# Kernel optimization log

Measured on AMD Instinct MI355X. Metric: run time of the kernel, lower is better.

Reference implementation:

```python
import jax, jax.numpy as jnp
import numpy as np

Q, N, FDIM, HDIM = 4096, 1024, 64, 128


def setup_inputs() -> dict:
    key = jax.random.key(0)
    ks = jax.random.split(key, 7)
    s = 0.05
    return {
        "query_points": jax.random.normal(ks[0], (Q, 3), dtype=jnp.float32),
        "node_features": jax.random.normal(ks[1], (N, FDIM), dtype=jnp.float32),
        "node_positions": jax.random.normal(ks[2], (N, 3), dtype=jnp.float32),
        # attention MLP: Linear(F+3 -> H), ReLU, Linear(H -> 1)
        "aW1": jax.random.normal(ks[3], (FDIM + 3, HDIM), dtype=jnp.float32) * s,
        "ab1": jnp.zeros((HDIM,), dtype=jnp.float32),
        "aW2": jax.random.normal(ks[4], (HDIM, 1), dtype=jnp.float32) * s,
        "ab2": jnp.zeros((1,), dtype=jnp.float32),
        # decoder MLP: Linear(F -> H), ReLU, Linear(H -> 3)
        "dW1": jax.random.normal(ks[5], (FDIM, HDIM), dtype=jnp.float32) * s,
        "db1": jnp.zeros((HDIM,), dtype=jnp.float32),
        "dW2": jax.random.normal(ks[6], (HDIM, 3), dtype=jnp.float32) * s,
        "db2": jnp.zeros((3,), dtype=jnp.float32),
    }


def reference(query_points, node_features, node_positions,
              aW1, ab1, aW2, ab2, dW1, db1, dW2, db2):
    F = node_features.shape[1]
    # pairwise offsets: [Q, N, 3]
    diff = query_points[:, None, :] - node_positions[None, :, :]
    # xy-plane distance -> inverse-distance weights: [Q, N, 1]
    dist = jnp.linalg.norm(diff[..., :2], axis=-1, keepdims=True)
    w = 1.0 / (dist + 1e-6)
    # attn MLP on concat([node_features, diff]); split W1 so the feature
    # part ([N,F]@[F,H]) is computed once instead of per query pair.
    h = jax.nn.relu(node_features @ aW1[:F] + diff @ aW1[F:] + ab1)  # [Q, N, H]
    score = h @ aW2 + ab2                                            # [Q, N, 1]
    attn = jax.nn.softmax(score * w, axis=1)                         # [Q, N, 1]
    agg = jnp.einsum('qn,nf->qf', attn[..., 0], node_features)       # [Q, F]
    return jax.nn.relu(agg @ dW1 + db1) @ dW2 + db2                  # [Q, 3]
```

## Files before the change

kernel.cpp:

```cpp
#include <hip/hip_runtime.h>
#include <math.h>

#define QN 4096
#define NN 1024
#define FD 64
#define HD 128

typedef float v2f __attribute__((ext_vector_type(2)));

#define OFF_UB    0
#define OFF_B     524288
#define OFF_VU    655360
#define OFF_VB    659456
#define OFF_L     660480
#define OFF_PM    4854784
#define OFF_PART  5116928
#define OFF_SPART 7214080

__global__ __launch_bounds__(256) void k0_prep(
    const float* __restrict__ qp, const float* __restrict__ nf,
    const float* __restrict__ npos, const float* __restrict__ aW1,
    const float* __restrict__ ab1, const float* __restrict__ aW2,
    float* __restrict__ B, float* __restrict__ UB,
    float* __restrict__ vu, float* __restrict__ vb) {
  int bid = blockIdx.x, t = threadIdx.x;
  if (bid < 2048) {
    int idx = bid * 256 + t;
    int e = idx & 1, lane = (idx >> 1) & 63, qq = (idx >> 7) & 3;
    int h2 = (idx >> 9) & 63, qblk = idx >> 15;
    int q = qblk * 256 + qq * 64 + lane;
    int h = h2 * 2 + e;
    float u = qp[q*3+0] * aW1[(FD+0)*HD + h]
            + qp[q*3+1] * aW1[(FD+1)*HD + h]
            + qp[q*3+2] * aW1[(FD+2)*HD + h];
    UB[idx] = u;
  } else if (bid < 2560) {
    int i2 = (bid - 2048) * 256 + t;
    int n = i2 >> 7, h = i2 & 127;
    float s = ab1[h];
    #pragma unroll
    for (int f = 0; f < FD; ++f) s = fmaf(nf[n*FD+f], aW1[f*HD+h], s);
    s -= npos[n*3+0] * aW1[(FD+0)*HD + h]
       + npos[n*3+1] * aW1[(FD+1)*HD + h]
       + npos[n*3+2] * aW1[(FD+2)*HD + h];
    B[i2] = s;
    float pv = s * aW2[h];
    #pragma unroll
    for (int m = 1; m < 64; m <<= 1) pv += __shfl_xor(pv, m, 64);
    __shared__ float ps[4];
    if ((t & 63) == 0) ps[t >> 6] = pv;
    __syncthreads();
    if (t == 0)   vb[n] = ps[0] + ps[1];
    if (t == 128) vb[n] = ps[2] + ps[3];
  } else {
    int q = (bid - 2560) * 256 + t;
    float q0 = qp[q*3+0], q1 = qp[q*3+1], q2 = qp[q*3+2];
    float acc = 0.f;
    #pragma unroll
    for (int h = 0; h < HD; ++h) {
      float u = q0 * aW1[(FD+0)*HD + h]
              + q1 * aW1[(FD+1)*HD + h]
              + q2 * aW1[(FD+2)*HD + h];
      acc = fmaf(aW2[h], u, acc);
    }
    vu[q] = acc;
  }
}


#define LOADU(dst) { \
  _Pragma("unroll") for (int qq = 0; qq < 4; ++qq) { \
    dst[qq][0] = P0[qq*64]; \
    dst[qq][1] = P0[qq*64 + 256]; \
    dst[qq][2] = P1[qq*64]; \
    dst[qq][3] = P1[qq*64 + 256]; } \
  P0 += 1024; P1 += 1024; }

#define COMPUTE(u) { \
  float aw0 = aw[0], aw1 = aw[1], aw2 = aw[2], aw3 = aw[3]; \
  float aw4 = aw[4], aw5 = aw[5], aw6 = aw[6], aw7 = aw[7]; \
  _Pragma("unroll") for (int nn = 0; nn < 4; ++nn) { \
    v2f b0 = bsB[nn*64], b1 = bsB[nn*64 + 1]; \
    v2f b2 = bsB[nn*64 + 2], b3 = bsB[nn*64 + 3]; \
    _Pragma("unroll") for (int qq = 0; qq < 4; ++qq) { \
      v2f t0 = u[qq][0] + b0; \
      v2f t1 = u[qq][1] + b1; \
      v2f t2 = u[qq][2] + b2; \
      v2f t3 = u[qq][3] + b3; \
      float a = acc[qq][nn]; \
      a = fmaf(aw0, __builtin_fabsf(t0.x), a); \
      a = fmaf(aw1, __builtin_fabsf(t0.y), a); \
      a = fmaf(aw2, __builtin_fabsf(t1.x), a); \
      a = fmaf(aw3, __builtin_fabsf(t1.y), a); \
      a = fmaf(aw4, __builtin_fabsf(t2.x), a); \
      a = fmaf(aw5, __builtin_fabsf(t2.y), a); \
      a = fmaf(aw6, __builtin_fabsf(t3.x), a); \
      a = fmaf(aw7, __builtin_fabsf(t3.y), a); \
      acc[qq][nn] = a; } } \
  bsB += 4; aw += 8; }

__global__ __launch_bounds__(256) void k2_logits(
    const float* __restrict__ Bg, const float* __restrict__ UB,
    const float* __restrict__ aW2, const float* __restrict__ ab2,
    const float* __restrict__ qp, const float* __restrict__ npos,
    const float* __restrict__ vu, const float* __restrict__ vb,
    float* __restrict__ L, float* __restrict__ pm) {
  __shared__ float Bs[16 * HD];
  __shared__ float red[4][4][64];
  const int q0 = blockIdx.x * 256, n0 = blockIdx.y * 16;
  const int t = threadIdx.x;
  {
    const float4* src = (const float4*)(Bg + n0 * HD);
    float4* dst = (float4*)Bs;
    #pragma unroll
    for (int r = 0; r < 2; ++r) dst[r*256 + t] = src[r*256 + t];
  }
  __syncthreads();
  const int lane = t & 63, w = t >> 6;
  const int nb = w * 4;

  float acc[4][4];
  #pragma unroll
  for (int qq = 0; qq < 4; ++qq)
    #pragma unroll
    for (int nn = 0; nn < 4; ++nn) acc[qq][nn] = 0.f;

  const v2f* P0 = (const v2f*)UB + (size_t)blockIdx.x * 16384 + lane;
  const v2f* P1 = P0 + 512;
  const v2f* bsB = (const v2f*)Bs + nb * 64;
  const float* aw = aW2;

  v2f uA[4][4], uB4[4][4];
  LOADU(uA);
  #pragma unroll 1
  for (int hc = 0; hc < 14; hc += 2) {
    LOADU(uB4);
    COMPUTE(uA);
    LOADU(uA);
    COMPUTE(uB4);
  }
  LOADU(uB4);
  COMPUTE(uA);
  COMPUTE(uB4);

  const float bias2 = ab2[0];
  float qx[4], qy[4], vuq[4], m4[4];
  #pragma unroll
  for (int qq = 0; qq < 4; ++qq) {
    int q = q0 + qq*64 + lane;
    qx[qq] = qp[q*3+0];
    qy[qq] = qp[q*3+1];
    vuq[qq] = vu[q];
    m4[qq] = -3.4e38f;
  }
  #pragma unroll
  for (int nn = 0; nn < 4; ++nn) {
    int n = n0 + nb + nn;
    float px = npos[n*3+0], py = npos[n*3+1];
    float vbn = vb[n];
    #pragma unroll
    for (int qq = 0; qq < 4; ++qq) {
      float dx = qx[qq] - px, dy = qy[qq] - py;
      float wgt = 1.f / (sqrtf(dx*dx + dy*dy) + 1e-6f);
      float score = fmaf(0.5f, vuq[qq] + vbn + acc[qq][nn], bias2);
      float lg = score * wgt;
      L[n * QN + q0 + qq*64 + lane] = lg;
      m4[qq] = fmaxf(m4[qq], lg);
    }
  }
  #pragma unroll
  for (int qq = 0; qq < 4; ++qq) red[w][qq][lane] = m4[qq];
  __syncthreads();
  {
    int qq = t >> 6, ll = t & 63;
    float mm = fmaxf(fmaxf(red[0][qq][ll], red[1][qq][ll]),
                     fmaxf(red[2][qq][ll], red[3][qq][ll]));
    pm[blockIdx.y * QN + q0 + qq*64 + ll] = mm;
  }
}

__global__ __launch_bounds__(256) void k4_agg(
    const float* __restrict__ L, const float* __restrict__ pm,
    const float* __restrict__ nf, float* __restrict__ part,
    float* __restrict__ spart) {
  __shared__ float red[4][2][32][33];
  __shared__ float sred[4][33];
  int b = blockIdx.x;
  int qt = b & 127, c = b >> 7;
  int t = threadIdx.x, lane = t & 63, w = t >> 6;
  int qi = lane & 31, fh = lane >> 5;
  int q = qt * 32 + qi;

  float m = -3.4e38f;
  #pragma unroll
  for (int k = 0; k < 64; ++k) m = fmaxf(m, pm[k * QN + q]);

  float acc[32];
  #pragma unroll
  for (int f = 0; f < 32; ++f) acc[f] = 0.f;
  float s = 0.f;

  int nbase = c * 128 + w * 32;
  const float* Lp = L + (size_t)nbase * QN + q;
  float cur = *Lp;
  for (int i = 0; i < 32; ++i) {
    float nxt = (i < 31) ? Lp[(size_t)(i + 1) * QN] : 0.f;
    float p = exp2f((cur - m) * 1.44269504088896f);
    s += p;
    const float4* nfr = (const float4*)(nf + (nbase + i) * FD + fh * 32);
    #pragma unroll
    for (int g = 0; g < 8; ++g) {
      float4 a = nfr[g];
      acc[g*4+0] = fmaf(p, a.x, acc[g*4+0]);
      acc[g*4+1] = fmaf(p, a.y, acc[g*4+1]);
      acc[g*4+2] = fmaf(p, a.z, acc[g*4+2]);
      acc[g*4+3] = fmaf(p, a.w, acc[g*4+3]);
    }
    cur = nxt;
  }

  #pragma unroll
  for (int fi = 0; fi < 32; ++fi) red[w][fh][fi][qi] = acc[fi];
  if (fh == 0) sred[w][qi] = s;
  __syncthreads();
  #pragma unroll
  for (int k = 0; k < 8; ++k) {
    int idx = k * 256 + t;
    int qq = idx >> 6, f = idx & 63;
    int f1 = f >> 5, f0 = f & 31;
    float sum = red[0][f1][f0][qq] + red[1][f1][f0][qq]
              + red[2][f1][f0][qq] + red[3][f1][f0][qq];
    part[((size_t)c * QN + qt*32 + qq) * 64 + f] = sum;
  }
  if (t < 32) {
    spart[c * QN + qt*32 + t] = sred[0][t] + sred[1][t] + sred[2][t] + sred[3][t];
  }
}

__global__ __launch_bounds__(256) void k5_dec(
    const float* __restrict__ part, const float* __restrict__ spart,
    const float* __restrict__ dW1, const float* __restrict__ db1,
    const float* __restrict__ dW2, const float* __restrict__ db2,
    float* __restrict__ out) {
  __shared__ float agg[16][64];
  __shared__ float inv[16];
  __shared__ float h1s[16][128];
  int t = threadIdx.x;
  int qb = blockIdx.x * 16;
  if (t < 16) {
    float s = 0.f;
    #pragma unroll
    for (int c = 0; c < 8; ++c) s += spart[c*QN + qb + t];
    inv[t] = 1.f / s;
  }
  {
    int f = t & 63, qh = t >> 6;
    #pragma unroll
    for (int pass = 0; pass < 4; ++pass) {
      int qs = pass*4 + qh;
      float v = 0.f;
      #pragma unroll
      for (int c = 0; c < 8; ++c) v += part[((size_t)c*QN + qb + qs)*64 + f];
      agg[qs][f] = v;
    }
  }
  __syncthreads();
  {
    int h = t & 127, qg = t >> 7;
    #pragma unroll
    for (int k = 0; k < 8; ++k) {
      int qs = qg*8 + k;
      float a = 0.f;
      #pragma unroll
      for (int f = 0; f < 64; ++f) a = fmaf(agg[qs][f], dW1[f*HD + h], a);
      h1s[qs][h] = fmaxf(a * inv[qs] + db1[h], 0.f);
    }
  }
  __syncthreads();
  if (t < 48) {
    int qs = t / 3, o = t % 3;
    float a = db2[o];
    #pragma unroll
    for (int h = 0; h < HD; ++h) a = fmaf(h1s[qs][h], dW2[h*3 + o], a);
    out[(qb + qs)*3 + o] = a;
  }
}

extern "C" void kernel_launch(void* const* d_in, const int* in_sizes, int n_in,
                              void* d_out, int out_size, void* d_ws, size_t ws_size,
                              hipStream_t stream) {
  const float* qp   = (const float*)d_in[0];
  const float* nf   = (const float*)d_in[1];
  const float* npos = (const float*)d_in[2];
  const float* aW1  = (const float*)d_in[3];
  const float* ab1  = (const float*)d_in[4];
  const float* aW2  = (const float*)d_in[5];
  const float* ab2  = (const float*)d_in[6];
  const float* dW1  = (const float*)d_in[7];
  const float* db1  = (const float*)d_in[8];
  const float* dW2  = (const float*)d_in[9];
  const float* db2  = (const float*)d_in[10];

  float* ws    = (float*)d_ws;
  float* UB    = ws + OFF_UB;
  float* B     = ws + OFF_B;
  float* vu    = ws + OFF_VU;
  float* vb    = ws + OFF_VB;
  float* L     = ws + OFF_L;
  float* pm    = ws + OFF_PM;
  float* part  = ws + OFF_PART;
  float* spart = ws + OFF_SPART;

  hipLaunchKernelGGL(k0_prep, dim3(2576), dim3(256), 0, stream,
                     qp, nf, npos, aW1, ab1, aW2, B, UB, vu, vb);
  hipLaunchKernelGGL(k2_logits, dim3(16, 64), dim3(256), 0, stream,
                     B, UB, aW2, ab2, qp, npos, vu, vb, L, pm);
  hipLaunchKernelGGL(k4_agg, dim3(1024), dim3(256), 0, stream, L, pm, nf, part, spart);
  hipLaunchKernelGGL(k5_dec, dim3(256), dim3(256), 0, stream,
                     part, spart, dW1, db1, dW2, db2, (float*)d_out);
}
```

Before: 104.3 us.

## Retile logits kernel to one query per thread with scalar B loads

The U table is re-laid out as h-pair-major over all queries. Each thread now owns one query and 16 nodes, instead of a 4x4 query-by-node tile fed from an LDS copy of B. B values are read directly from global memory at wave-uniform addresses, which the compiler can turn into scalar loads, removing the LDS staging, the syncthreads and the cross-wave max reduction. This trades B reuse across the query tile for cheaper broadcast loads, and each thread reads U for only one query per h step instead of four.

New measurement: 107.3 us. 2.8% more time.

```diff
diff --git a/kernel.cpp b/kernel.cpp
--- a/kernel.cpp
+++ b/kernel.cpp
@@ -8,7 +8,7 @@
 
 typedef float v2f __attribute__((ext_vector_type(2)));
 
-#define OFF_UB    0
+#define OFF_UT2   0
 #define OFF_B     524288
 #define OFF_VU    655360
 #define OFF_VB    659456
@@ -21,19 +21,17 @@
     const float* __restrict__ qp, const float* __restrict__ nf,
     const float* __restrict__ npos, const float* __restrict__ aW1,
     const float* __restrict__ ab1, const float* __restrict__ aW2,
-    float* __restrict__ B, float* __restrict__ UB,
+    float* __restrict__ B, float* __restrict__ UT2,
     float* __restrict__ vu, float* __restrict__ vb) {
   int bid = blockIdx.x, t = threadIdx.x;
   if (bid < 2048) {
     int idx = bid * 256 + t;
-    int e = idx & 1, lane = (idx >> 1) & 63, qq = (idx >> 7) & 3;
-    int h2 = (idx >> 9) & 63, qblk = idx >> 15;
-    int q = qblk * 256 + qq * 64 + lane;
+    int e = idx & 1, q = (idx >> 1) & 4095, h2 = idx >> 13;
     int h = h2 * 2 + e;
     float u = qp[q*3+0] * aW1[(FD+0)*HD + h]
             + qp[q*3+1] * aW1[(FD+1)*HD + h]
             + qp[q*3+2] * aW1[(FD+2)*HD + h];
-    UB[idx] = u;
+    UT2[idx] = u;
   } else if (bid < 2560) {
     int i2 = (bid - 2048) * 256 + t;
     int n = i2 >> 7, h = i2 & 127;
@@ -67,116 +65,74 @@
   }
 }
 
-
-#define LOADU(dst) { \
-  _Pragma("unroll") for (int qq = 0; qq < 4; ++qq) { \
-    dst[qq][0] = P0[qq*64]; \
-    dst[qq][1] = P0[qq*64 + 256]; \
-    dst[qq][2] = P1[qq*64]; \
-    dst[qq][3] = P1[qq*64 + 256]; } \
-  P0 += 1024; P1 += 1024; }
-
-#define COMPUTE(u) { \
-  float aw0 = aw[0], aw1 = aw[1], aw2 = aw[2], aw3 = aw[3]; \
-  float aw4 = aw[4], aw5 = aw[5], aw6 = aw[6], aw7 = aw[7]; \
-  _Pragma("unroll") for (int nn = 0; nn < 4; ++nn) { \
-    v2f b0 = bsB[nn*64], b1 = bsB[nn*64 + 1]; \
-    v2f b2 = bsB[nn*64 + 2], b3 = bsB[nn*64 + 3]; \
-    _Pragma("unroll") for (int qq = 0; qq < 4; ++qq) { \
-      v2f t0 = u[qq][0] + b0; \
-      v2f t1 = u[qq][1] + b1; \
-      v2f t2 = u[qq][2] + b2; \
-      v2f t3 = u[qq][3] + b3; \
-      float a = acc[qq][nn]; \
-      a = fmaf(aw0, __builtin_fabsf(t0.x), a); \
-      a = fmaf(aw1, __builtin_fabsf(t0.y), a); \
-      a = fmaf(aw2, __builtin_fabsf(t1.x), a); \
-      a = fmaf(aw3, __builtin_fabsf(t1.y), a); \
-      a = fmaf(aw4, __builtin_fabsf(t2.x), a); \
-      a = fmaf(aw5, __builtin_fabsf(t2.y), a); \
-      a = fmaf(aw6, __builtin_fabsf(t3.x), a); \
-      a = fmaf(aw7, __builtin_fabsf(t3.y), a); \
-      acc[qq][nn] = a; } } \
-  bsB += 4; aw += 8; }
-
 __global__ __launch_bounds__(256) void k2_logits(
-    const float* __restrict__ Bg, const float* __restrict__ UB,
+    const float* __restrict__ Bg, const float* __restrict__ UT2,
     const float* __restrict__ aW2, const float* __restrict__ ab2,
     const float* __restrict__ qp, const float* __restrict__ npos,
     const float* __restrict__ vu, const float* __restrict__ vb,
     float* __restrict__ L, float* __restrict__ pm) {
-  __shared__ float Bs[16 * HD];
-  __shared__ float red[4][4][64];
-  const int q0 = blockIdx.x * 256, n0 = blockIdx.y * 16;
   const int t = threadIdx.x;
-  {
-    const float4* src = (const float4*)(Bg + n0 * HD);
-    float4* dst = (float4*)Bs;
-    #pragma unroll
-    for (int r = 0; r < 2; ++r) dst[r*256 + t] = src[r*256 + t];
-  }
-  __syncthreads();
   const int lane = t & 63, w = t >> 6;
-  const int nb = w * 4;
-
-  float acc[4][4];
-  #pragma unroll
-  for (int qq = 0; qq < 4; ++qq)
-    #pragma unroll
-    for (int nn = 0; nn < 4; ++nn) acc[qq][nn] = 0.f;
-
-  const v2f* P0 = (const v2f*)UB + (size_t)blockIdx.x * 16384 + lane;
-  const v2f* P1 = P0 + 512;
-  const v2f* bsB = (const v2f*)Bs + nb * 64;
-  const float* aw = aW2;
-
-  v2f uA[4][4], uB4[4][4];
-  LOADU(uA);
+  const int q = blockIdx.x * 256 + w * 64 + lane;
+  const int n0 = blockIdx.y * 16;
+
+  float acc[16];
+  #pragma unroll
+  for (int nn = 0; nn < 16; ++nn) acc[nn] = 0.f;
+
+  const v2f* up = (const v2f*)UT2 + q;
+
+  v2f uc[4], un[4];
+  #pragma unroll
+  for (int p = 0; p < 4; ++p) uc[p] = up[p * 4096];
+
   #pragma unroll 1
-  for (int hc = 0; hc < 14; hc += 2) {
-    LOADU(uB4);
-    COMPUTE(uA);
-    LOADU(uA);
-    COMPUTE(uB4);
-  }
-  LOADU(uB4);
-  COMPUTE(uA);
-  COMPUTE(uB4);
+  for (int hc = 0; hc < 16; ++hc) {
+    if (hc < 15) {
+      const v2f* upn = up + (hc + 1) * 4 * 4096;
+      #pragma unroll
+      for (int p = 0; p < 4; ++p) un[p] = upn[p * 4096];
+    }
+    const float* awp = aW2 + hc * 8;
+    float aw0 = awp[0], aw1 = awp[1], aw2 = awp[2], aw3 = awp[3];
+    float aw4 = awp[4], aw5 = awp[5], aw6 = awp[6], aw7 = awp[7];
+    #pragma unroll
+    for (int nn = 0; nn < 16; ++nn) {
+      const float* bp = Bg + (n0 + nn) * HD + hc * 8;
+      float b0 = bp[0], b1 = bp[1], b2 = bp[2], b3 = bp[3];
+      float b4 = bp[4], b5 = bp[5], b6 = bp[6], b7 = bp[7];
+      float a = acc[nn];
+      a = fmaf(aw0, __builtin_fabsf(uc[0].x + b0), a);
+      a = fmaf(aw1, __builtin_fabsf(uc[0].y + b1), a);
+      a = fmaf(aw2, __builtin_fabsf(uc[1].x + b2), a);
+      a = fmaf(aw3, __builtin_fabsf(uc[1].y + b3), a);
+      a = fmaf(aw4, __builtin_fabsf(uc[2].x + b4), a);
+      a = fmaf(aw5, __builtin_fabsf(uc[2].y + b5), a);
+      a = fmaf(aw6, __builtin_fabsf(uc[3].x + b6), a);
+      a = fmaf(aw7, __builtin_fabsf(uc[3].y + b7), a);
+      acc[nn] = a;
+    }
+    #pragma unroll
+    for (int p = 0; p < 4; ++p) uc[p] = un[p];
+  }
 
   const float bias2 = ab2[0];
-  float qx[4], qy[4], vuq[4], m4[4];
-  #pragma unroll
-  for (int qq = 0; qq < 4; ++qq) {
-    int q = q0 + qq*64 + lane;
-    qx[qq] = qp[q*3+0];
-    qy[qq] = qp[q*3+1];
-    vuq[qq] = vu[q];
-    m4[qq] = -3.4e38f;
-  }
-  #pragma unroll
-  for (int nn = 0; nn < 4; ++nn) {
-    int n = n0 + nb + nn;
+  const float qx = qp[q*3+0], qy = qp[q*3+1];
+  const float vuq = vu[q];
+  float m = -3.4e38f;
+  #pragma unroll
+  for (int nn = 0; nn < 16; ++nn) {
+    int n = n0 + nn;
     float px = npos[n*3+0], py = npos[n*3+1];
     float vbn = vb[n];
-    #pragma unroll
-    for (int qq = 0; qq < 4; ++qq) {
-      float dx = qx[qq] - px, dy = qy[qq] - py;
-      float wgt = 1.f / (sqrtf(dx*dx + dy*dy) + 1e-6f);
-      float score = fmaf(0.5f, vuq[qq] + vbn + acc[qq][nn], bias2);
-      float lg = score * wgt;
-      L[n * QN + q0 + qq*64 + lane] = lg;
-      m4[qq] = fmaxf(m4[qq], lg);
-    }
-  }
-  #pragma unroll
-  for (int qq = 0; qq < 4; ++qq) red[w][qq][lane] = m4[qq];
-  __syncthreads();
-  {
-    int qq = t >> 6, ll = t & 63;
-    float mm = fmaxf(fmaxf(red[0][qq][ll], red[1][qq][ll]),
-                     fmaxf(red[2][qq][ll], red[3][qq][ll]));
-    pm[blockIdx.y * QN + q0 + qq*64 + ll] = mm;
-  }
+    float dx = qx - px, dy = qy - py;
+    float wgt = 1.f / (sqrtf(dx*dx + dy*dy) + 1e-6f);
+    float score = fmaf(0.5f, vuq + vbn + acc[nn], bias2);
+    float lg = score * wgt;
+    L[n * QN + q] = lg;
+    m = fmaxf(m, lg);
+  }
+  pm[blockIdx.y * QN + q] = m;
 }
 
 __global__ __launch_bounds__(256) void k4_agg(
@@ -302,7 +258,7 @@
   const float* db2  = (const float*)d_in[10];
 
   float* ws    = (float*)d_ws;
-  float* UB    = ws + OFF_UB;
+  float* UT2   = ws + OFF_UT2;
   float* B     = ws + OFF_B;
   float* vu    = ws + OFF_VU;
   float* vb    = ws + OFF_VB;
@@ -312,9 +268,9 @@
   float* spart = ws + OFF_SPART;
 
   hipLaunchKernelGGL(k0_prep, dim3(2576), dim3(256), 0, stream,
-                     qp, nf, npos, aW1, ab1, aW2, B, UB, vu, vb);
+                     qp, nf, npos, aW1, ab1, aW2, B, UT2, vu, vb);
   hipLaunchKernelGGL(k2_logits, dim3(16, 64), dim3(256), 0, stream,
-                     B, UB, aW2, ab2, qp, npos, vu, vb, L, pm);
+                     B, UT2, aW2, ab2, qp, npos, vu, vb, L, pm);
   hipLaunchKernelGGL(k4_agg, dim3(1024), dim3(256), 0, stream, L, pm, nf, part, spart);
   hipLaunchKernelGGL(k5_dec, dim3(256), dim3(256), 0, stream,
                      part, spart, dW1, db1, dW2, db2, (float*)d_out);
```

## Repack query projection as h4-major float4 layout and deepen logit prefetch

Applied to the files above, without the earlier changes.

Changes the per-query projection buffer to a layout with four consecutive hidden units per float4, so the logits kernel issues 16-byte loads instead of 8-byte ones and reads B from shared memory as float4. Packed adds are emitted through inline v_pk_add_f32 asm, and the aW2 values are now read per use instead of cached in locals. The aggregation kernel now prefetches logits four rows ahead instead of one to hide global-load latency. Risks include more register pressure, and the inline asm may block compiler scheduling.

Result: no change. 105.0 us (+0.6%).

```diff
diff --git a/kernel.cpp b/kernel.cpp
--- a/kernel.cpp
+++ b/kernel.cpp
@@ -7,8 +7,9 @@
 #define HD 128
 
 typedef float v2f __attribute__((ext_vector_type(2)));
-
-#define OFF_UB    0
+typedef float v4f __attribute__((ext_vector_type(4)));
+
+#define OFF_UT4   0
 #define OFF_B     524288
 #define OFF_VU    655360
 #define OFF_VB    659456
@@ -21,19 +22,17 @@
     const float* __restrict__ qp, const float* __restrict__ nf,
     const float* __restrict__ npos, const float* __restrict__ aW1,
     const float* __restrict__ ab1, const float* __restrict__ aW2,
-    float* __restrict__ B, float* __restrict__ UB,
+    float* __restrict__ B, float* __restrict__ UT4,
     float* __restrict__ vu, float* __restrict__ vb) {
   int bid = blockIdx.x, t = threadIdx.x;
   if (bid < 2048) {
     int idx = bid * 256 + t;
-    int e = idx & 1, lane = (idx >> 1) & 63, qq = (idx >> 7) & 3;
-    int h2 = (idx >> 9) & 63, qblk = idx >> 15;
-    int q = qblk * 256 + qq * 64 + lane;
-    int h = h2 * 2 + e;
+    int j = idx & 3, q = (idx >> 2) & 4095, h4 = idx >> 14;
+    int h = h4 * 4 + j;
     float u = qp[q*3+0] * aW1[(FD+0)*HD + h]
             + qp[q*3+1] * aW1[(FD+1)*HD + h]
             + qp[q*3+2] * aW1[(FD+2)*HD + h];
-    UB[idx] = u;
+    UT4[idx] = u;
   } else if (bid < 2560) {
     int i2 = (bid - 2048) * 256 + t;
     int n = i2 >> 7, h = i2 & 127;
@@ -67,40 +66,44 @@
   }
 }
 
-
 #define LOADU(dst) { \
   _Pragma("unroll") for (int qq = 0; qq < 4; ++qq) { \
-    dst[qq][0] = P0[qq*64]; \
-    dst[qq][1] = P0[qq*64 + 256]; \
-    dst[qq][2] = P1[qq*64]; \
-    dst[qq][3] = P1[qq*64 + 256]; } \
-  P0 += 1024; P1 += 1024; }
+    dst[qq][0] = p0[qq*64]; \
+    dst[qq][1] = p1[qq*64]; } \
+  p0 += 8192; p1 += 8192; }
 
 #define COMPUTE(u) { \
-  float aw0 = aw[0], aw1 = aw[1], aw2 = aw[2], aw3 = aw[3]; \
-  float aw4 = aw[4], aw5 = aw[5], aw6 = aw[6], aw7 = aw[7]; \
   _Pragma("unroll") for (int nn = 0; nn < 4; ++nn) { \
-    v2f b0 = bsB[nn*64], b1 = bsB[nn*64 + 1]; \
-    v2f b2 = bsB[nn*64 + 2], b3 = bsB[nn*64 + 3]; \
+    v4f b0 = bsb[(nb + nn)*32]; \
+    v4f b1 = bsb[(nb + nn)*32 + 1]; \
+    v2f b01 = __builtin_shufflevector(b0, b0, 0, 1); \
+    v2f b23 = __builtin_shufflevector(b0, b0, 2, 3); \
+    v2f b45 = __builtin_shufflevector(b1, b1, 0, 1); \
+    v2f b67 = __builtin_shufflevector(b1, b1, 2, 3); \
     _Pragma("unroll") for (int qq = 0; qq < 4; ++qq) { \
-      v2f t0 = u[qq][0] + b0; \
-      v2f t1 = u[qq][1] + b1; \
-      v2f t2 = u[qq][2] + b2; \
-      v2f t3 = u[qq][3] + b3; \
+      v2f u01 = __builtin_shufflevector(u[qq][0], u[qq][0], 0, 1); \
+      v2f u23 = __builtin_shufflevector(u[qq][0], u[qq][0], 2, 3); \
+      v2f u45 = __builtin_shufflevector(u[qq][1], u[qq][1], 0, 1); \
+      v2f u67 = __builtin_shufflevector(u[qq][1], u[qq][1], 2, 3); \
+      v2f t0, t1, t2, t3; \
+      asm("v_pk_add_f32 %0, %1, %2" : "=v"(t0) : "v"(u01), "v"(b01)); \
+      asm("v_pk_add_f32 %0, %1, %2" : "=v"(t1) : "v"(u23), "v"(b23)); \
+      asm("v_pk_add_f32 %0, %1, %2" : "=v"(t2) : "v"(u45), "v"(b45)); \
+      asm("v_pk_add_f32 %0, %1, %2" : "=v"(t3) : "v"(u67), "v"(b67)); \
       float a = acc[qq][nn]; \
-      a = fmaf(aw0, __builtin_fabsf(t0.x), a); \
-      a = fmaf(aw1, __builtin_fabsf(t0.y), a); \
-      a = fmaf(aw2, __builtin_fabsf(t1.x), a); \
-      a = fmaf(aw3, __builtin_fabsf(t1.y), a); \
-      a = fmaf(aw4, __builtin_fabsf(t2.x), a); \
-      a = fmaf(aw5, __builtin_fabsf(t2.y), a); \
-      a = fmaf(aw6, __builtin_fabsf(t3.x), a); \
-      a = fmaf(aw7, __builtin_fabsf(t3.y), a); \
+      a = fmaf(aw[0], __builtin_fabsf(t0.x), a); \
+      a = fmaf(aw[1], __builtin_fabsf(t0.y), a); \
+      a = fmaf(aw[2], __builtin_fabsf(t1.x), a); \
+      a = fmaf(aw[3], __builtin_fabsf(t1.y), a); \
+      a = fmaf(aw[4], __builtin_fabsf(t2.x), a); \
+      a = fmaf(aw[5], __builtin_fabsf(t2.y), a); \
+      a = fmaf(aw[6], __builtin_fabsf(t3.x), a); \
+      a = fmaf(aw[7], __builtin_fabsf(t3.y), a); \
       acc[qq][nn] = a; } } \
-  bsB += 4; aw += 8; }
+  bsb += 2; aw += 8; }
 
 __global__ __launch_bounds__(256) void k2_logits(
-    const float* __restrict__ Bg, const float* __restrict__ UB,
+    const float* __restrict__ Bg, const float* __restrict__ UT4,
     const float* __restrict__ aW2, const float* __restrict__ ab2,
     const float* __restrict__ qp, const float* __restrict__ npos,
     const float* __restrict__ vu, const float* __restrict__ vb,
@@ -125,12 +128,12 @@
     #pragma unroll
     for (int nn = 0; nn < 4; ++nn) acc[qq][nn] = 0.f;
 
-  const v2f* P0 = (const v2f*)UB + (size_t)blockIdx.x * 16384 + lane;
-  const v2f* P1 = P0 + 512;
-  const v2f* bsB = (const v2f*)Bs + nb * 64;
+  const v4f* p0 = (const v4f*)UT4 + q0 + lane;
+  const v4f* p1 = p0 + 4096;
+  const v4f* bsb = (const v4f*)Bs;
   const float* aw = aW2;
 
-  v2f uA[4][4], uB4[4][4];
+  v4f uA[4][2], uB4[4][2];
   LOADU(uA);
   #pragma unroll 1
   for (int hc = 0; hc < 14; hc += 2) {
@@ -202,9 +205,15 @@
 
   int nbase = c * 128 + w * 32;
   const float* Lp = L + (size_t)nbase * QN + q;
-  float cur = *Lp;
+
+  float pre[4];
+  #pragma unroll
+  for (int j = 0; j < 4; ++j) pre[j] = Lp[(size_t)j * QN];
+
+  #pragma unroll 4
   for (int i = 0; i < 32; ++i) {
-    float nxt = (i < 31) ? Lp[(size_t)(i + 1) * QN] : 0.f;
+    float cur = pre[i & 3];
+    if (i < 28) pre[i & 3] = Lp[(size_t)(i + 4) * QN];
     float p = exp2f((cur - m) * 1.44269504088896f);
     s += p;
     const float4* nfr = (const float4*)(nf + (nbase + i) * FD + fh * 32);
@@ -216,7 +225,6 @@
       acc[g*4+2] = fmaf(p, a.z, acc[g*4+2]);
       acc[g*4+3] = fmaf(p, a.w, acc[g*4+3]);
     }
-    cur = nxt;
   }
 
   #pragma unroll
@@ -302,7 +310,7 @@
   const float* db2  = (const float*)d_in[10];
 
   float* ws    = (float*)d_ws;
-  float* UB    = ws + OFF_UB;
+  float* UT4   = ws + OFF_UT4;
   float* B     = ws + OFF_B;
   float* vu    = ws + OFF_VU;
   float* vb    = ws + OFF_VB;
@@ -312,9 +320,9 @@
   float* spart = ws + OFF_SPART;
 
   hipLaunchKernelGGL(k0_prep, dim3(2576), dim3(256), 0, stream,
-                     qp, nf, npos, aW1, ab1, aW2, B, UB, vu, vb);
+                     qp, nf, npos, aW1, ab1, aW2, B, UT4, vu, vb);
   hipLaunchKernelGGL(k2_logits, dim3(16, 64), dim3(256), 0, stream,
-                     B, UB, aW2, ab2, qp, npos, vu, vb, L, pm);
+                     B, UT4, aW2, ab2, qp, npos, vu, vb, L, pm);
   hipLaunchKernelGGL(k4_agg, dim3(1024), dim3(256), 0, stream, L, pm, nf, part, spart);
   hipLaunchKernelGGL(k5_dec, dim3(256), dim3(256), 0, stream,
                      part, spart, dW1, db1, dW2, db2, (float*)d_out);
```
